# Kernel optimization log

Measured on AMD Instinct MI355X. Metric: run time of the kernel, lower is better.

Reference implementation:

```python
import jax, jax.numpy as jnp
import numpy as np

N_NODES = 50000   # total nodes across the batch of graphs
N_EDGES = 800000  # avg degree 16
F_IN = 128        # num_features
DIM = 256         # hidden dim
N_LAYERS = 3      # num_gc_layers
N_GRAPHS = 512    # graphs in the batch (max(batch)+1)
BN_EPS = 1e-5


def setup_inputs() -> dict:
    key = jax.random.key(0)
    ks = jax.random.split(key, 16)
    inp = {}
    inp["x"] = jax.random.normal(ks[0], (N_NODES, F_IN), dtype=jnp.float32)
    inp["edge_index"] = jax.random.randint(ks[1], (2, N_EDGES), 0, N_NODES, dtype=jnp.int64)
    inp["batch"] = jnp.sort(jax.random.randint(ks[2], (N_NODES,), 0, N_GRAPHS, dtype=jnp.int64))
    k = 3
    for i in range(N_LAYERS):
        fin = F_IN if i == 0 else DIM
        inp[f"w1_{i}"] = jax.random.normal(ks[k], (fin, DIM), dtype=jnp.float32) / np.sqrt(fin); k += 1
        inp[f"b1_{i}"] = jnp.zeros((DIM,), dtype=jnp.float32)
        inp[f"w2_{i}"] = jax.random.normal(ks[k], (DIM, DIM), dtype=jnp.float32) / np.sqrt(DIM); k += 1
        inp[f"b2_{i}"] = jnp.zeros((DIM,), dtype=jnp.float32)
        inp[f"bn_g{i}"] = jnp.ones((DIM,), dtype=jnp.float32)
        inp[f"bn_b{i}"] = jnp.zeros((DIM,), dtype=jnp.float32)
    return inp


def _gin_layer(h, src, dst, w1, b1, w2, b2, g, b):
    # GINConv (eps=0): agg_i = h_i + sum_{j->i} h_j  (scatter-add over edges)
    agg = h + jax.ops.segment_sum(h[src], dst, num_segments=N_NODES)
    # MLP: Linear -> ReLU -> Linear
    m = jnp.maximum(agg @ w1 + b1, 0.0) @ w2 + b2
    # F.relu then BatchNorm1d (training mode: batch statistics, biased var)
    m = jnp.maximum(m, 0.0)
    mu = m.mean(axis=0)
    var = ((m - mu) ** 2).mean(axis=0)
    return g * (m - mu) / jnp.sqrt(var + BN_EPS) + b


def reference(x, edge_index, batch,
              w1_0, b1_0, w2_0, b2_0, bn_g0, bn_b0,
              w1_1, b1_1, w2_1, b2_1, bn_g1, bn_b1,
              w1_2, b1_2, w2_2, b2_2, bn_g2, bn_b2):
    src, dst = edge_index[0], edge_index[1]
    params = [
        (w1_0, b1_0, w2_0, b2_0, bn_g0, bn_b0),
        (w1_1, b1_1, w2_1, b2_1, bn_g1, bn_b1),
        (w1_2, b1_2, w2_2, b2_2, bn_g2, bn_b2),
    ]
    xs = []
    h = x
    for p in params:
        h = _gin_layer(h, src, dst, *p)
        xs.append(h)
    # global add-pool readout per layer, concat along feature dim
    pooled = jnp.concatenate(
        [jax.ops.segment_sum(hi, batch, num_segments=N_GRAPHS) for hi in xs], axis=1)
    return pooled, jnp.concatenate(xs, axis=1)
```

## Files before the change

kernel.cpp:

```cpp
#include <hip/hip_runtime.h>

#define N_NODES 50000
#define N_EDGES 800000
#define F_IN 128
#define DIM 256
#define N_GRAPHS 512
#define BN_EPS 1e-5f

typedef unsigned short u16;
typedef unsigned int u32;
using floatx4 = __attribute__((ext_vector_type(4))) float;
using short8 = __attribute__((ext_vector_type(8))) short;

__device__ __forceinline__ u16 f2b(float f) {
    u32 u = __float_as_uint(f);
    return (u16)((u + 0x7fffu + ((u >> 16) & 1u)) >> 16);
}
__device__ __forceinline__ float blo(u32 u) { return __uint_as_float(u << 16); }
__device__ __forceinline__ float bhi(u32 u) { return __uint_as_float(u & 0xffff0000u); }
__device__ __forceinline__ u32 pack2(float a, float b) {
    return (u32)f2b(a) | ((u32)f2b(b) << 16);
}
__device__ __forceinline__ void load_lds16(const void* g, void* l) {
    __builtin_amdgcn_global_load_lds((const __attribute__((address_space(1))) void*)g,
                                     (__attribute__((address_space(3))) void*)l, 16, 0, 0);
}


__global__ void count_deg(const int* __restrict__ dst, int* __restrict__ deg, int nE) {
    int e = blockIdx.x * 256 + threadIdx.x;
    if (e < nE) atomicAdd(&deg[dst[e]], 1);
}

__global__ void scan_block(const int* __restrict__ deg, int* __restrict__ row_start,
                           int* __restrict__ bsum, int n) {
    __shared__ int wtot[4];
    int i = blockIdx.x * 256 + threadIdx.x;
    int lane = threadIdx.x & 63, w = threadIdx.x >> 6;
    int v = (i < n) ? deg[i] : 0;
    int s = v;
#pragma unroll
    for (int d = 1; d < 64; d <<= 1) {
        int t = __shfl_up(s, d);
        if (lane >= d) s += t;
    }
    if (lane == 63) wtot[w] = s;
    __syncthreads();
    int off = 0;
#pragma unroll
    for (int k = 0; k < 4; ++k)
        if (k < w) off += wtot[k];
    s += off;
    if (i < n) row_start[i + 1] = s;
    if (threadIdx.x == 255) bsum[blockIdx.x] = s;
}

__global__ void scan_partials(const int* __restrict__ bsum, int* __restrict__ boff,
                              int* __restrict__ row_start, int* __restrict__ cursor, int nb) {
    __shared__ int wtot[4];
    int i = threadIdx.x;
    int lane = i & 63, w = i >> 6;
    int v = (i < nb) ? bsum[i] : 0;
    int s = v;
#pragma unroll
    for (int d = 1; d < 64; d <<= 1) {
        int t = __shfl_up(s, d);
        if (lane >= d) s += t;
    }
    if (lane == 63) wtot[w] = s;
    __syncthreads();
    int off = 0;
#pragma unroll
    for (int k = 0; k < 4; ++k)
        if (k < w) off += wtot[k];
    boff[i] = s + off - v;
    if (i == 0) { row_start[0] = 0; cursor[0] = 0; }
}

__global__ void add_offsets(int* __restrict__ row_start, int* __restrict__ cursor,
                            const int* __restrict__ boff, int n) {
    int i = blockIdx.x * 256 + threadIdx.x;
    if (i < n) {
        int fin = row_start[i + 1] + boff[blockIdx.x];
        row_start[i + 1] = fin;
        cursor[i + 1] = fin;
    }
}

__global__ void fill_csr(const int* __restrict__ src, const int* __restrict__ dst,
                         int* __restrict__ cursor, int* __restrict__ srcs, int nE) {
    int e = blockIdx.x * 256 + threadIdx.x;
    if (e < nE) {
        int p = atomicAdd(&cursor[dst[e]], 1);
        srcs[p] = src[e];
    }
}


__global__ void convert_all(const float4* __restrict__ x4, uint2* __restrict__ Hout, int n4,
                            const float* __restrict__ w10, const float* __restrict__ w11,
                            const float* __restrict__ w12, const float* __restrict__ w20,
                            const float* __restrict__ w21, const float* __restrict__ w22,
                            u16* __restrict__ Wall) {
    int i = blockIdx.x * 256 + threadIdx.x;
    if (i < n4) {
        float4 v = x4[i];
        uint2 p;
        p.x = pack2(v.x, v.y);
        p.y = pack2(v.z, v.w);
        Hout[i] = p;
        return;
    }
    int j = i - n4;
    if (j >= 360448) return;
    const float* w;
    int K, base;
    if (j < 32768)       { w = w10; K = 128; base = 0; }
    else if (j < 98304)  { w = w11; K = 256; base = 32768; }
    else if (j < 163840) { w = w12; K = 256; base = 98304; }
    else if (j < 229376) { w = w20; K = 256; base = 163840; }
    else if (j < 294912) { w = w21; K = 256; base = 229376; }
    else                 { w = w22; K = 256; base = 294912; }
    int loc = j - base;
    int nn = loc / K, kk = loc - nn * K;
    Wall[j] = f2b(w[(size_t)kk * 256 + nn]);
}


template <int F>
__global__ void aggregate_bf16(const u16* __restrict__ h, const int* __restrict__ row_start,
                               const int* __restrict__ srcs, u16* __restrict__ outp, int n) {
    constexpr int NWD = F / 128;
    int node = (int)(((size_t)blockIdx.x * blockDim.x + threadIdx.x) >> 6);
    int lane = threadIdx.x & 63;
    if (node >= n) return;
    const u32* base = (const u32*)h;
    int cw = lane * NWD;
    float acc[2 * NWD];
#pragma unroll
    for (int t = 0; t < NWD; ++t) {
        u32 v0 = base[(size_t)node * (F / 2) + cw + t];
        acc[2 * t] = blo(v0);
        acc[2 * t + 1] = bhi(v0);
    }
    int s = row_start[node], e = row_start[node + 1];
    for (int j0 = s; j0 < e; j0 += 64) {
        int myidx = (j0 + lane < e) ? srcs[j0 + lane] : 0;
        int cnt = min(64, e - j0);
        int j = 0;
        for (; j + 7 < cnt; j += 8) {
            u32 a[8][NWD];
#pragma unroll
            for (int q = 0; q < 8; ++q) {
                int sq = __shfl(myidx, j + q);
#pragma unroll
                for (int t = 0; t < NWD; ++t) a[q][t] = base[(size_t)sq * (F / 2) + cw + t];
            }
#pragma unroll
            for (int q = 0; q < 8; ++q)
#pragma unroll
                for (int t = 0; t < NWD; ++t) {
                    acc[2 * t] += blo(a[q][t]);
                    acc[2 * t + 1] += bhi(a[q][t]);
                }
        }
        for (; j + 3 < cnt; j += 4) {
            u32 a[4][NWD];
#pragma unroll
            for (int q = 0; q < 4; ++q) {
                int sq = __shfl(myidx, j + q);
#pragma unroll
                for (int t = 0; t < NWD; ++t) a[q][t] = base[(size_t)sq * (F / 2) + cw + t];
            }
#pragma unroll
            for (int q = 0; q < 4; ++q)
#pragma unroll
                for (int t = 0; t < NWD; ++t) {
                    acc[2 * t] += blo(a[q][t]);
                    acc[2 * t + 1] += bhi(a[q][t]);
                }
        }
        for (; j < cnt; ++j) {
            int s0 = __shfl(myidx, j);
            u32 a0[NWD];
#pragma unroll
            for (int t = 0; t < NWD; ++t) a0[t] = base[(size_t)s0 * (F / 2) + cw + t];
#pragma unroll
            for (int t = 0; t < NWD; ++t) {
                acc[2 * t] += blo(a0[t]);
                acc[2 * t + 1] += bhi(a0[t]);
            }
        }
    }
    u32* op = (u32*)outp;
#pragma unroll
    for (int t = 0; t < NWD; ++t)
        op[(size_t)node * (F / 2) + cw + t] = pack2(acc[2 * t], acc[2 * t + 1]);
}


template <int MODE>
__global__ __launch_bounds__(512) void gemm_mfma(
    const u16* __restrict__ A, const u16* __restrict__ Bt, const float* __restrict__ bias,
    void* __restrict__ Cout, float* __restrict__ sums, int M, int K) {
    __shared__ u16 As[128 * 32];
    __shared__ u16 Bs[256 * 32];
    const int tid = threadIdx.x;
    const int w = tid >> 6, lane = tid & 63;
    const int wm = w >> 2, wn = w & 3;
    const int r = lane & 15, rg = lane >> 4;
    const int bm = blockIdx.x * 128;

    floatx4 acc[4][4];
#pragma unroll
    for (int i = 0; i < 4; ++i)
#pragma unroll
        for (int j = 0; j < 4; ++j) acc[i][j] = (floatx4){0.f, 0.f, 0.f, 0.f};

    for (int k0 = 0; k0 < K; k0 += 32) {
        __syncthreads();
        {
            int arow = bm + (tid >> 2);
            if (arow >= M) arow = M - 1;
            load_lds16(A + (size_t)arow * K + k0 + (tid & 3) * 8, As + w * 512);
#pragma unroll
            for (int q = 0; q < 2; ++q) {
                int i = q * 512 + tid;
                int nrow = i >> 2;
                load_lds16(Bt + (size_t)nrow * K + k0 + (i & 3) * 8, Bs + (q * 8 + w) * 512);
            }
        }
        __syncthreads();
        short8 a[4], b[4];
#pragma unroll
        for (int mi = 0; mi < 4; ++mi)
            a[mi] = *(const short8*)(As + (wm * 64 + mi * 16 + r) * 32 + rg * 8);
#pragma unroll
        for (int ni = 0; ni < 4; ++ni)
            b[ni] = *(const short8*)(Bs + (wn * 64 + ni * 16 + r) * 32 + rg * 8);
#pragma unroll
        for (int mi = 0; mi < 4; ++mi)
#pragma unroll
            for (int ni = 0; ni < 4; ++ni)
                acc[mi][ni] = __builtin_amdgcn_mfma_f32_16x16x32_bf16(a[mi], b[ni], acc[mi][ni], 0, 0, 0);
    }

    if (MODE == 0) {
        u16* C = (u16*)Cout;
#pragma unroll
        for (int ni = 0; ni < 4; ++ni) {
            int col = wn * 64 + ni * 16 + r;
            float bv = bias[col];
#pragma unroll
            for (int mi = 0; mi < 4; ++mi)
#pragma unroll
                for (int rr = 0; rr < 4; ++rr) {
                    int row = bm + wm * 64 + mi * 16 + rg * 4 + rr;
                    if (row < M) C[(size_t)row * 256 + col] = f2b(fmaxf(acc[mi][ni][rr] + bv, 0.f));
                }
        }
    } else {
        float* C = (float*)Cout;
#pragma unroll
        for (int ni = 0; ni < 4; ++ni) {
            int col = wn * 64 + ni * 16 + r;
            float bv = bias[col];
            float s = 0.f, s2 = 0.f;
#pragma unroll
            for (int mi = 0; mi < 4; ++mi)
#pragma unroll
                for (int rr = 0; rr < 4; ++rr) {
                    int row = bm + wm * 64 + mi * 16 + rg * 4 + rr;
                    if (row < M) {
                        float v = fmaxf(acc[mi][ni][rr] + bv, 0.f);
                        C[(size_t)row * 256 + col] = v;
                        s += v;
                        s2 += v * v;
                    }
                }
            s += __shfl_xor(s, 16);
            s += __shfl_xor(s, 32);
            s2 += __shfl_xor(s2, 16);
            s2 += __shfl_xor(s2, 32);
            if (rg == 0) {
                atomicAdd(&sums[col], s);
                atomicAdd(&sums[256 + col], s2);
            }
        }
    }
}


template <int WRITE_H>
__global__ void bn_apply_pool(const float* __restrict__ Mfp, const float* __restrict__ sums,
                              const float* __restrict__ g, const float* __restrict__ bb,
                              const int* __restrict__ batch, float* __restrict__ out_nodes,
                              u16* __restrict__ H, float* __restrict__ pooled,
                              int col_off, int n, float inv_n) {
    int w = threadIdx.x >> 6, lane = threadIdx.x & 63;
    int base = blockIdx.x * 64 + w * 16;
    if (base >= n) return;
    int c4 = lane << 2;
    float4 s1 = *(const float4*)(sums + c4);
    float4 s2 = *(const float4*)(sums + 256 + c4);
    float4 g4 = *(const float4*)(g + c4);
    float4 b4 = *(const float4*)(bb + c4);
    float4 sc, sh;
    {
        float mux = s1.x * inv_n, muy = s1.y * inv_n, muz = s1.z * inv_n, muw = s1.w * inv_n;
        sc.x = g4.x / sqrtf(s2.x * inv_n - mux * mux + BN_EPS);
        sc.y = g4.y / sqrtf(s2.y * inv_n - muy * muy + BN_EPS);
        sc.z = g4.z / sqrtf(s2.z * inv_n - muz * muz + BN_EPS);
        sc.w = g4.w / sqrtf(s2.w * inv_n - muw * muw + BN_EPS);
        sh.x = b4.x - mux * sc.x;
        sh.y = b4.y - muy * sc.y;
        sh.z = b4.z - muz * sc.z;
        sh.w = b4.w - muw * sc.w;
    }
    float4 acc = make_float4(0.f, 0.f, 0.f, 0.f);
    int gcur = -1;
    int end = min(base + 16, n);
    for (int row = base; row < end; ++row) {
        float4 v = *(const float4*)(Mfp + (size_t)row * 256 + c4);
        float4 o;
        o.x = fmaf(v.x, sc.x, sh.x);
        o.y = fmaf(v.y, sc.y, sh.y);
        o.z = fmaf(v.z, sc.z, sh.z);
        o.w = fmaf(v.w, sc.w, sh.w);
        *(float4*)(out_nodes + (size_t)row * 768 + col_off + c4) = o;
        if (WRITE_H) {
            uint2 pk;
            pk.x = pack2(o.x, o.y);
            pk.y = pack2(o.z, o.w);
            *(uint2*)(H + (size_t)row * 256 + c4) = pk;
        }
        int gg = batch[row];
        if (gg != gcur) {
            if (gcur >= 0) {
                float* pp = pooled + (size_t)gcur * 768 + col_off + c4;
                atomicAdd(pp + 0, acc.x);
                atomicAdd(pp + 1, acc.y);
                atomicAdd(pp + 2, acc.z);
                atomicAdd(pp + 3, acc.w);
            }
            gcur = gg;
            acc = o;
        } else {
            acc.x += o.x; acc.y += o.y; acc.z += o.z; acc.w += o.w;
        }
    }
    if (gcur >= 0) {
        float* pp = pooled + (size_t)gcur * 768 + col_off + c4;
        atomicAdd(pp + 0, acc.x);
        atomicAdd(pp + 1, acc.y);
        atomicAdd(pp + 2, acc.z);
        atomicAdd(pp + 3, acc.w);
    }
}


extern "C" void kernel_launch(void* const* d_in, const int* in_sizes, int n_in,
                              void* d_out, int out_size, void* d_ws, size_t ws_size,
                              hipStream_t stream) {
    const float* x = (const float*)d_in[0];
    const int* esrc = (const int*)d_in[1];
    const int* edst = esrc + N_EDGES;
    const int* batch = (const int*)d_in[2];

    const float* w1[3] = {(const float*)d_in[3], (const float*)d_in[9], (const float*)d_in[15]};
    const float* b1[3] = {(const float*)d_in[4], (const float*)d_in[10], (const float*)d_in[16]};
    const float* w2[3] = {(const float*)d_in[5], (const float*)d_in[11], (const float*)d_in[17]};
    const float* b2[3] = {(const float*)d_in[6], (const float*)d_in[12], (const float*)d_in[18]};
    const float* bng[3] = {(const float*)d_in[7], (const float*)d_in[13], (const float*)d_in[19]};
    const float* bnb[3] = {(const float*)d_in[8], (const float*)d_in[14], (const float*)d_in[20]};

    float* out_pooled = (float*)d_out;
    float* out_nodes = (float*)d_out + (size_t)N_GRAPHS * 768;

    char* p = (char*)d_ws;
    float* Mfp = (float*)p;
    u16* Abf = (u16*)p;
    p += (size_t)N_NODES * 256 * 4;
    u16* T = (u16*)p;  p += (size_t)N_NODES * 256 * 2;
    u16* H = (u16*)p;  p += (size_t)N_NODES * 256 * 2;
    u16* Wall = (u16*)p; p += (size_t)360448 * 2;
    float* sums = (float*)p; p += 3 * 512 * 4;
    int* deg = (int*)p;      p += (size_t)N_NODES * 4;
    const size_t zero_bytes = 3 * 512 * 4 + (size_t)N_NODES * 4;
    int* row_start = (int*)p; p += (size_t)(N_NODES + 1) * 4;
    int* cursor = (int*)p;    p += (size_t)(N_NODES + 1) * 4;
    int* srcs = (int*)p;      p += (size_t)N_EDGES * 4;
    int* bsum = (int*)p;      p += 256 * 4;
    int* boff = (int*)p;      p += 256 * 4;

    const u16* W1t[3] = {Wall, Wall + 32768, Wall + 98304};
    const u16* W2t[3] = {Wall + 163840, Wall + 229376, Wall + 294912};

    const int NBLK = (N_NODES + 255) / 256;

    hipMemsetAsync(sums, 0, zero_bytes, stream);
    hipMemsetAsync(out_pooled, 0, (size_t)N_GRAPHS * 768 * sizeof(float), stream);

    count_deg<<<(N_EDGES + 255) / 256, 256, 0, stream>>>(edst, deg, N_EDGES);
    scan_block<<<NBLK, 256, 0, stream>>>(deg, row_start, bsum, N_NODES);
    scan_partials<<<1, 256, 0, stream>>>(bsum, boff, row_start, cursor, NBLK);
    add_offsets<<<NBLK, 256, 0, stream>>>(row_start, cursor, boff, N_NODES);
    fill_csr<<<(N_EDGES + 255) / 256, 256, 0, stream>>>(esrc, edst, cursor, srcs, N_EDGES);

    {
        const int n4 = N_NODES * F_IN / 4;
        const int tot = n4 + 360448;
        convert_all<<<(tot + 255) / 256, 256, 0, stream>>>(
            (const float4*)x, (uint2*)H, n4,
            w1[0], w1[1], w1[2], w2[0], w2[1], w2[2], Wall);
    }

    const int GGRID = (N_NODES + 127) / 128;
    const int PBLK = (N_NODES + 63) / 64;
    for (int L = 0; L < 3; ++L) {
        int K1 = (L == 0) ? F_IN : DIM;
        float* sumsL = sums + L * 512;
        if (L == 0)
            aggregate_bf16<128><<<(N_NODES + 3) / 4, 256, 0, stream>>>(H, row_start, srcs, Abf, N_NODES);
        else
            aggregate_bf16<256><<<(N_NODES + 3) / 4, 256, 0, stream>>>(H, row_start, srcs, Abf, N_NODES);
        gemm_mfma<0><<<GGRID, 512, 0, stream>>>(Abf, W1t[L], b1[L], (void*)T, nullptr, N_NODES, K1);
        gemm_mfma<1><<<GGRID, 512, 0, stream>>>(T, W2t[L], b2[L], (void*)Mfp, sumsL, N_NODES, DIM);
        if (L < 2)
            bn_apply_pool<1><<<PBLK, 256, 0, stream>>>(Mfp, sumsL, bng[L], bnb[L], batch,
                                                       out_nodes, H, out_pooled, L * 256, N_NODES, 1.0f / N_NODES);
        else
            bn_apply_pool<0><<<PBLK, 256, 0, stream>>>(Mfp, sumsL, bng[L], bnb[L], batch,
                                                       out_nodes, H, out_pooled, L * 256, N_NODES, 1.0f / N_NODES);
    }
}
```

Before: 725.3 us.

## Fuse neighbor aggregation into first MLP GEMM via LDS-staged aggregated tile

Replaces the separate aggregation kernel and first GEMM with one kernel. Each block gathers and sums neighbor features for 64 nodes into a swizzled LDS tile, then runs the bf16 MFMA GEMM with bias and ReLU directly from that tile. This removes the write and re-read of the aggregated activation buffer and one launch per layer. In exchange the GEMM tile shrinks to 64 rows, the gather phase is serialized per wave (16 nodes each) before any MFMA work, and occupancy is limited by a 32 KB LDS tile.

```diff
diff --git a/kernel.cpp b/kernel.cpp
--- a/kernel.cpp
+++ b/kernel.cpp
@@ -127,75 +127,154 @@
 }
 
 
-template <int F>
-__global__ void aggregate_bf16(const u16* __restrict__ h, const int* __restrict__ row_start,
-                               const int* __restrict__ srcs, u16* __restrict__ outp, int n) {
-    constexpr int NWD = F / 128;
-    int node = (int)(((size_t)blockIdx.x * blockDim.x + threadIdx.x) >> 6);
-    int lane = threadIdx.x & 63;
-    if (node >= n) return;
-    const u32* base = (const u32*)h;
-    int cw = lane * NWD;
-    float acc[2 * NWD];
-#pragma unroll
-    for (int t = 0; t < NWD; ++t) {
-        u32 v0 = base[(size_t)node * (F / 2) + cw + t];
-        acc[2 * t] = blo(v0);
-        acc[2 * t + 1] = bhi(v0);
-    }
-    int s = row_start[node], e = row_start[node + 1];
-    for (int j0 = s; j0 < e; j0 += 64) {
-        int myidx = (j0 + lane < e) ? srcs[j0 + lane] : 0;
-        int cnt = min(64, e - j0);
-        int j = 0;
-        for (; j + 7 < cnt; j += 8) {
-            u32 a[8][NWD];
-#pragma unroll
-            for (int q = 0; q < 8; ++q) {
-                int sq = __shfl(myidx, j + q);
-#pragma unroll
-                for (int t = 0; t < NWD; ++t) a[q][t] = base[(size_t)sq * (F / 2) + cw + t];
+template <int K>
+__global__ __launch_bounds__(256, 3) void agg_gemm1(
+    const u16* __restrict__ H, const int* __restrict__ row_start, const int* __restrict__ srcs,
+    const u16* __restrict__ Bt, const float* __restrict__ bias,
+    u16* __restrict__ Cout, int M) {
+    __shared__ u16 Ap[64 * K];
+    __shared__ u16 Bs[256 * 32];
+    const int tid = threadIdx.x;
+    const int w = tid >> 6, lane = tid & 63;
+    const int r = lane & 15, rg = lane >> 4;
+    const int bm = blockIdx.x * 64;
+    constexpr int RB = K * 2;
+
+    for (int rr = 0; rr < 16; ++rr) {
+        int m = w * 16 + rr;
+        int node = bm + m;
+        if (node >= M) node = M - 1;
+        if constexpr (K == 256) {
+            const uint2* hb = (const uint2*)H;
+            uint2 v = hb[(size_t)node * 64 + lane];
+            float a0 = blo(v.x), a1 = bhi(v.x), a2 = blo(v.y), a3 = bhi(v.y);
+            int s = row_start[node], e = row_start[node + 1];
+            for (int j0 = s; j0 < e; j0 += 64) {
+                int myidx = (j0 + lane < e) ? srcs[j0 + lane] : 0;
+                int cnt = min(64, e - j0);
+                int j = 0;
+                for (; j + 7 < cnt; j += 8) {
+                    uint2 g[8];
+#pragma unroll
+                    for (int q = 0; q < 8; ++q) {
+                        int sq = __shfl(myidx, j + q);
+                        g[q] = hb[(size_t)sq * 64 + lane];
+                    }
+#pragma unroll
+                    for (int q = 0; q < 8; ++q) {
+                        a0 += blo(g[q].x); a1 += bhi(g[q].x);
+                        a2 += blo(g[q].y); a3 += bhi(g[q].y);
+                    }
+                }
+                for (; j + 3 < cnt; j += 4) {
+                    uint2 g[4];
+#pragma unroll
+                    for (int q = 0; q < 4; ++q) {
+                        int sq = __shfl(myidx, j + q);
+                        g[q] = hb[(size_t)sq * 64 + lane];
+                    }
+#pragma unroll
+                    for (int q = 0; q < 4; ++q) {
+                        a0 += blo(g[q].x); a1 += bhi(g[q].x);
+                        a2 += blo(g[q].y); a3 += bhi(g[q].y);
+                    }
+                }
+                for (; j < cnt; ++j) {
+                    int sq = __shfl(myidx, j);
+                    uint2 g0 = hb[(size_t)sq * 64 + lane];
+                    a0 += blo(g0.x); a1 += bhi(g0.x);
+                    a2 += blo(g0.y); a3 += bhi(g0.y);
+                }
             }
-#pragma unroll
-            for (int q = 0; q < 8; ++q)
-#pragma unroll
-                for (int t = 0; t < NWD; ++t) {
-                    acc[2 * t] += blo(a[q][t]);
-                    acc[2 * t + 1] += bhi(a[q][t]);
-                }
-        }
-        for (; j + 3 < cnt; j += 4) {
-            u32 a[4][NWD];
-#pragma unroll
-            for (int q = 0; q < 4; ++q) {
-                int sq = __shfl(myidx, j + q);
-#pragma unroll
-                for (int t = 0; t < NWD; ++t) a[q][t] = base[(size_t)sq * (F / 2) + cw + t];
+            int ck = (lane >> 1) ^ (m & 7);
+            char* lp = (char*)Ap + m * RB + (ck << 4) + (lane & 1) * 8;
+            *(uint2*)lp = make_uint2(pack2(a0, a1), pack2(a2, a3));
+        } else {
+            const u32* hb = (const u32*)H;
+            u32 v = hb[(size_t)node * 64 + lane];
+            float a0 = blo(v), a1 = bhi(v);
+            int s = row_start[node], e = row_start[node + 1];
+            for (int j0 = s; j0 < e; j0 += 64) {
+                int myidx = (j0 + lane < e) ? srcs[j0 + lane] : 0;
+                int cnt = min(64, e - j0);
+                int j = 0;
+                for (; j + 7 < cnt; j += 8) {
+                    u32 g[8];
+#pragma unroll
+                    for (int q = 0; q < 8; ++q) {
+                        int sq = __shfl(myidx, j + q);
+                        g[q] = hb[(size_t)sq * 64 + lane];
+                    }
+#pragma unroll
+                    for (int q = 0; q < 8; ++q) { a0 += blo(g[q]); a1 += bhi(g[q]); }
+                }
+                for (; j + 3 < cnt; j += 4) {
+                    u32 g[4];
+#pragma unroll
+                    for (int q = 0; q < 4; ++q) {
+                        int sq = __shfl(myidx, j + q);
+                        g[q] = hb[(size_t)sq * 64 + lane];
+                    }
+#pragma unroll
+                    for (int q = 0; q < 4; ++q) { a0 += blo(g[q]); a1 += bhi(g[q]); }
+                }
+                for (; j < cnt; ++j) {
+                    int sq = __shfl(myidx, j);
+                    u32 g0 = hb[(size_t)sq * 64 + lane];
+                    a0 += blo(g0); a1 += bhi(g0);
+                }
             }
-#pragma unroll
-            for (int q = 0; q < 4; ++q)
-#pragma unroll
-                for (int t = 0; t < NWD; ++t) {
-                    acc[2 * t] += blo(a[q][t]);
-                    acc[2 * t + 1] += bhi(a[q][t]);
-                }
-        }
-        for (; j < cnt; ++j) {
-            int s0 = __shfl(myidx, j);
-            u32 a0[NWD];
-#pragma unroll
-            for (int t = 0; t < NWD; ++t) a0[t] = base[(size_t)s0 * (F / 2) + cw + t];
-#pragma unroll
-            for (int t = 0; t < NWD; ++t) {
-                acc[2 * t] += blo(a0[t]);
-                acc[2 * t + 1] += bhi(a0[t]);
+            int ck = (lane >> 2) ^ (m & 7);
+            char* lp = (char*)Ap + m * RB + (ck << 4) + (lane & 3) * 4;
+            *(u32*)lp = pack2(a0, a1);
+        }
+    }
+
+    floatx4 acc[4][4];
+#pragma unroll
+    for (int i = 0; i < 4; ++i)
+#pragma unroll
+        for (int j = 0; j < 4; ++j) acc[i][j] = (floatx4){0.f, 0.f, 0.f, 0.f};
+
+    for (int k0 = 0; k0 < K; k0 += 32) {
+        __syncthreads();
+#pragma unroll
+        for (int q = 0; q < 4; ++q) {
+            int i = q * 256 + tid;
+            int nrow = i >> 2;
+            load_lds16(Bt + (size_t)nrow * K + k0 + (i & 3) * 8, Bs + (q * 4 + w) * 512);
+        }
+        __syncthreads();
+        short8 a[4], b[4];
+#pragma unroll
+        for (int mi = 0; mi < 4; ++mi) {
+            int m = mi * 16 + r;
+            int ck = ((k0 >> 3) + rg) ^ (m & 7);
+            a[mi] = *(const short8*)((const char*)Ap + m * RB + (ck << 4));
+        }
+#pragma unroll
+        for (int ni = 0; ni < 4; ++ni)
+            b[ni] = *(const short8*)(Bs + (w * 64 + ni * 16 + r) * 32 + rg * 8);
+#pragma unroll
+        for (int mi = 0; mi < 4; ++mi)
+#pragma unroll
+            for (int ni = 0; ni < 4; ++ni)
+                acc[mi][ni] = __builtin_amdgcn_mfma_f32_16x16x32_bf16(a[mi], b[ni], acc[mi][ni], 0, 0, 0);
+    }
+
+    u16* C = (u16*)Cout;
+#pragma unroll
+    for (int ni = 0; ni < 4; ++ni) {
+        int col = w * 64 + ni * 16 + r;
+        float bv = bias[col];
+#pragma unroll
+        for (int mi = 0; mi < 4; ++mi)
+#pragma unroll
+            for (int rr2 = 0; rr2 < 4; ++rr2) {
+                int row = bm + mi * 16 + rg * 4 + rr2;
+                if (row < M) C[(size_t)row * 256 + col] = f2b(fmaxf(acc[mi][ni][rr2] + bv, 0.f));
             }
-        }
-    }
-    u32* op = (u32*)outp;
-#pragma unroll
-    for (int t = 0; t < NWD; ++t)
-        op[(size_t)node * (F / 2) + cw + t] = pack2(acc[2 * t], acc[2 * t + 1]);
+    }
 }
 
 
@@ -379,7 +458,6 @@
 
     char* p = (char*)d_ws;
     float* Mfp = (float*)p;
-    u16* Abf = (u16*)p;
     p += (size_t)N_NODES * 256 * 4;
     u16* T = (u16*)p;  p += (size_t)N_NODES * 256 * 2;
     u16* H = (u16*)p;  p += (size_t)N_NODES * 256 * 2;
@@ -415,16 +493,15 @@
             w1[0], w1[1], w1[2], w2[0], w2[1], w2[2], Wall);
     }
 
+    const int FGRID = (N_NODES + 63) / 64;
     const int GGRID = (N_NODES + 127) / 128;
     const int PBLK = (N_NODES + 63) / 64;
     for (int L = 0; L < 3; ++L) {
-        int K1 = (L == 0) ? F_IN : DIM;
         float* sumsL = sums + L * 512;
         if (L == 0)
-            aggregate_bf16<128><<<(N_NODES + 3) / 4, 256, 0, stream>>>(H, row_start, srcs, Abf, N_NODES);
+            agg_gemm1<128><<<FGRID, 256, 0, stream>>>(H, row_start, srcs, W1t[L], b1[L], T, N_NODES);
         else
-            aggregate_bf16<256><<<(N_NODES + 3) / 4, 256, 0, stream>>>(H, row_start, srcs, Abf, N_NODES);
-        gemm_mfma<0><<<GGRID, 512, 0, stream>>>(Abf, W1t[L], b1[L], (void*)T, nullptr, N_NODES, K1);
+            agg_gemm1<256><<<FGRID, 256, 0, stream>>>(H, row_start, srcs, W1t[L], b1[L], T, N_NODES);
         gemm_mfma<1><<<GGRID, 512, 0, stream>>>(T, W2t[L], b2[L], (void*)Mfp, sumsL, N_NODES, DIM);
         if (L < 2)
             bn_apply_pool<1><<<PBLK, 256, 0, stream>>>(Mfp, sumsL, bng[L], bnb[L], batch,
```

After: 818.9 us. +12.9%, slower.
